# Performance work log

Measured on AMD Instinct MI355X. Metric: run time of the kernel, lower is better.

## Reference

```python
import jax, jax.numpy as jnp
import numpy as np

REG_MAX = 16
BOX_W = 7.5
OBJ_W = 1.0
TOPK = 10
EPS = 1e-7


def dfl_decode(x, reg_max):
    # x: [B, 4*reg_max, N] -> expected value of per-side distribution -> [B, N, 4] (xyxy)
    B, C, N = x.shape
    x = x.reshape(B, 4, reg_max, N)
    p = jax.nn.softmax(x, axis=2)
    proj = jnp.arange(reg_max, dtype=x.dtype)
    return jnp.einsum('bkrn,r->bnk', p, proj)


def bbox_ciou(b1, b2):
    # b1: [B,N,1,4], b2: [B,1,M,4], xyxy -> [B,N,M]
    x11, y11, x12, y12 = b1[..., 0], b1[..., 1], b1[..., 2], b1[..., 3]
    x21, y21, x22, y22 = b2[..., 0], b2[..., 1], b2[..., 2], b2[..., 3]
    w1, h1 = x12 - x11, y12 - y11
    w2, h2 = x22 - x21, y22 - y21
    iw = jnp.clip(jnp.minimum(x12, x22) - jnp.maximum(x11, x21), 0.0)
    ih = jnp.clip(jnp.minimum(y12, y22) - jnp.maximum(y11, y21), 0.0)
    inter = iw * ih
    union = w1 * h1 + w2 * h2 - inter + EPS
    iou = inter / union
    cw = jnp.maximum(x12, x22) - jnp.minimum(x11, x21)
    ch = jnp.maximum(y12, y22) - jnp.minimum(y11, y21)
    c2 = cw * cw + ch * ch + EPS
    rho2 = ((x21 + x22 - x11 - x12) ** 2 + (y21 + y22 - y11 - y12) ** 2) * 0.25
    v = (4.0 / (np.pi ** 2)) * (jnp.arctan(w2 / (h2 + EPS)) - jnp.arctan(w1 / (h1 + EPS))) ** 2
    alpha = jax.lax.stop_gradient(v / (v - iou + 1.0 + EPS))
    return iou - rho2 / c2 - alpha * v


def setup_inputs() -> dict:
    key = jax.random.key(0)
    k1, k2, k3, k4 = jax.random.split(key, 4)
    B, N, M = 8, 34000, 64
    boxes = jax.random.normal(k1, (B, 4 * REG_MAX, N), dtype=jnp.float32)
    scores = jax.random.normal(k2, (B, N), dtype=jnp.float32)
    # GT boxes: valid xyxy in roughly the same [0, reg_max) range as decoded preds
    xy = jax.random.uniform(k3, (B, M, 2), dtype=jnp.float32) * 11.0
    wh = jax.random.uniform(k4, (B, M, 2), dtype=jnp.float32) * 4.0 + 0.5
    targets = jnp.concatenate([xy, xy + wh], axis=-1)
    return {'boxes': boxes, 'scores': scores, 'targets': targets}


def reference(boxes, scores, targets):
    B, N = scores.shape
    M = targets.shape[1]
    pb = dfl_decode(boxes, REG_MAX)                     # [B,N,4]
    ciou = bbox_ciou(pb[:, :, None, :], targets[:, None, :, :])  # [B,N,M]
    k = min(TOPK, N)
    topv, topi = jax.lax.top_k(jnp.swapaxes(ciou, 1, 2), k)      # [B,M,k] over anchors
    valid = topv > 0.0
    vals = jnp.where(valid, topv, 0.0)

    def per_batch(idx, val, vld):
        flat_i = idx.reshape(-1)
        iou_t = jnp.zeros((N,), val.dtype).at[flat_i].max(val.reshape(-1))
        pos = jnp.zeros((N,), bool).at[flat_i].max(vld.reshape(-1))
        return iou_t, pos

    iou_target, pos = jax.vmap(per_batch)(topi, vals, valid)     # [B,N]
    posf = pos.astype(iou_target.dtype)
    npos = posf.sum(axis=1)
    box_per = jnp.where(npos > 0,
                        ((1.0 - iou_target) * posf).sum(axis=1) / jnp.maximum(npos, 1.0),
                        0.0)
    box_loss = box_per.sum()
    # BCEWithLogits (mean over anchors), summed over batch
    bce = jnp.maximum(scores, 0.0) - scores * iou_target + jnp.log1p(jnp.exp(-jnp.abs(scores)))
    obj_loss = bce.mean(axis=1).sum()
    total = (BOX_W * box_loss + OBJ_W * obj_loss) / B
    return total, box_loss, obj_loss
```

## Files before the change

kernel.cpp:

```cpp
#include <hip/hip_runtime.h>
#include <math.h>

#define BQ 8
#define MQ 64
#define REGMAX 16
#define KTOP 10
#define EPSQ 1e-7f
#define MBUF 1344

__device__ __forceinline__ float frcp(float x) { return __builtin_amdgcn_rcpf(x); }

#define ST_BYTES 256

__global__ __launch_bounds__(256) void decode_topk_kernel(
    const float* __restrict__ boxes, const float* __restrict__ scores,
    const float* __restrict__ targets, unsigned int* __restrict__ iou_bits,
    uint2* __restrict__ cand, float* __restrict__ acc, int N, int bpb) {
  const int tid = threadIdx.x;
  const int b = blockIdx.x / bpb;
  const int blk = blockIdx.x - b * bpb;
  const int a0 = blk * 256;
  const int w = tid >> 6;
  const int l = tid & 63;

  __shared__ float s_r1[5120];
  __shared__ float s_r2[1664];
  __shared__ int s_cnt;
  __shared__ float s_bce;
  float* stage = s_r1;
  float* s_hv = s_r1;
  int* s_hi = (int*)(s_r1 + 2560);
  float4* s_sv = (float4*)s_r2;
  float* s_at = s_r2 + 1024;
  int* s_ix = (int*)(s_r2 + 1280);
  uint2* s_mg = (uint2*)s_r2;

  if (tid == 0) { s_cnt = 0; s_bce = 0.f; }

  float out[4];
  const int c4 = a0 + l * 4;
  const bool cok = (c4 < N);
#pragma unroll
  for (int k = 0; k < 4; ++k) {
#pragma unroll
    for (int i = 0; i < 4; ++i) {
      const int r = w + i * 4;
      float4 v = make_float4(0.f, 0.f, 0.f, 0.f);
      if (cok)
        v = *(const float4*)&boxes[(size_t)(b * 64 + k * 16 + r) * (size_t)N + c4];
      *(float4*)&stage[r * 256 + l * 4] = v;
    }
    __syncthreads();
    float x[REGMAX];
#pragma unroll
    for (int r = 0; r < REGMAX; ++r) x[r] = stage[r * 256 + tid];
    float mx = x[0];
#pragma unroll
    for (int r = 1; r < REGMAX; ++r) mx = fmaxf(mx, x[r]);
    float s = 0.f, ws = 0.f;
#pragma unroll
    for (int r = 0; r < REGMAX; ++r) {
      float e = __expf(x[r] - mx);
      s += e;
      ws += (float)r * e;
    }
    out[k] = ws * frcp(s);
    __syncthreads();
  }

  const int n = a0 + tid;
  float bce0 = 0.f;
  if (n < N) {
    const size_t i = (size_t)b * N + n;
    iou_bits[i] = 0u;
    float sc = scores[i];
    bce0 = fmaxf(sc, 0.f) + log1pf(__expf(-fabsf(sc)));
    float x1 = out[0], y1 = out[1], x2 = out[2], y2 = out[3];
    float w1 = x2 - x1, h1 = y2 - y1;
    if (w1 > 0.f && h1 > 0.f) {
      int slot = atomicAdd(&s_cnt, 1);
      s_sv[slot] = make_float4(x1, y1, x2, y2);
      s_at[slot] = atanf(w1 * frcp(h1 + EPSQ));
      s_ix[slot] = n;
    }
  }
#pragma unroll
  for (int d = 1; d < 64; d <<= 1) bce0 += __shfl_xor(bce0, d, 64);
  if (l == 0) atomicAdd(&s_bce, bce0);
  __syncthreads();
  const int nsurv = s_cnt;
  if (tid == 0) atomicAdd(&acc[b * 4 + 2], s_bce);

  const float4 t = ((const float4*)targets)[b * MQ + l];
  const float x21 = t.x, y21 = t.y, x22 = t.z, y22 = t.w;
  const float w2 = x22 - x21, h2 = y22 - y21;
  const float atan_t = atanf(w2 * frcp(h2 + EPSQ));
  const float area2 = w2 * h2, sumx2 = x21 + x22, sumy2 = y21 + y22;
  const float CPI = 4.0f / (float)(M_PI * M_PI);

  float hv0 = 0.f, hv1 = 0.f, hv2 = 0.f, hv3 = 0.f, hv4 = 0.f;
  float hv5 = 0.f, hv6 = 0.f, hv7 = 0.f, hv8 = 0.f, hv9 = 0.f;
  int hi0 = 0, hi1 = 0, hi2 = 0, hi3 = 0, hi4 = 0;
  int hi5 = 0, hi6 = 0, hi7 = 0, hi8 = 0, hi9 = 0;

  const int qlen = (nsurv + 3) >> 2;
  const int j0 = w * qlen;
  const int j1 = min(nsurv, j0 + qlen);
  for (int j = j0; j < j1; ++j) {
    float4 p = s_sv[j];
    float pa = s_at[j];
    int ixj = s_ix[j];
    float x11 = p.x, y11 = p.y, x12 = p.z, y12 = p.w;
    float w1 = x12 - x11, h1 = y12 - y11;
    float iw = fmaxf(fminf(x12, x22) - fmaxf(x11, x21), 0.f);
    float ih = fmaxf(fminf(y12, y22) - fmaxf(y11, y21), 0.f);
    float inter = iw * ih;
    float uni = w1 * h1 + area2 - inter + EPSQ;
    float iou = inter * frcp(uni);
    float cw = fmaxf(x12, x22) - fminf(x11, x21);
    float ch = fmaxf(y12, y22) - fminf(y11, y21);
    float c2 = cw * cw + ch * ch + EPSQ;
    float dx = sumx2 - x11 - x12;
    float dy = sumy2 - y11 - y12;
    float rho2 = (dx * dx + dy * dy) * 0.25f;
    float da = atan_t - pa;
    float v = CPI * da * da;
    float alpha = v * frcp(v - iou + 1.f + EPSQ);
    float ciou = iou - rho2 * frcp(c2) - alpha * v;
    if (ciou > hv9) {
      float cv = ciou;
      int ci = ixj;
#define INS(vk, ik)                         \
  {                                         \
    bool gt = cv > vk;                      \
    float tv_ = vk; int ti_ = ik;           \
    vk = gt ? cv : vk; ik = gt ? ci : ik;   \
    cv = gt ? tv_ : cv; ci = gt ? ti_ : ci; \
  }
      INS(hv0, hi0) INS(hv1, hi1) INS(hv2, hi2) INS(hv3, hi3) INS(hv4, hi4)
      INS(hv5, hi5) INS(hv6, hi6) INS(hv7, hi7) INS(hv8, hi8) INS(hv9, hi9)
#undef INS
    }
  }
  const int hb = (w * MQ + l) * KTOP;
  s_hv[hb + 0] = hv0; s_hi[hb + 0] = hi0;
  s_hv[hb + 1] = hv1; s_hi[hb + 1] = hi1;
  s_hv[hb + 2] = hv2; s_hi[hb + 2] = hi2;
  s_hv[hb + 3] = hv3; s_hi[hb + 3] = hi3;
  s_hv[hb + 4] = hv4; s_hi[hb + 4] = hi4;
  s_hv[hb + 5] = hv5; s_hi[hb + 5] = hi5;
  s_hv[hb + 6] = hv6; s_hi[hb + 6] = hi6;
  s_hv[hb + 7] = hv7; s_hi[hb + 7] = hi7;
  s_hv[hb + 8] = hv8; s_hi[hb + 8] = hi8;
  s_hv[hb + 9] = hv9; s_hi[hb + 9] = hi9;
  __syncthreads();

  if (w == 0) {
    const int m = l;
    int p0 = 0, p1 = 0, p2 = 0, p3 = 0;
    for (int r = 0; r < KTOP; ++r) {
      float c0 = s_hv[(0 * MQ + m) * KTOP + p0];
      float c1 = s_hv[(1 * MQ + m) * KTOP + p1];
      float c2m = s_hv[(2 * MQ + m) * KTOP + p2];
      float c3 = s_hv[(3 * MQ + m) * KTOP + p3];
      float best = c0; int bw = 0;
      if (c1 > best) { best = c1; bw = 1; }
      if (c2m > best) { best = c2m; bw = 2; }
      if (c3 > best) { best = c3; bw = 3; }
      int psel = (bw == 0) ? p0 : (bw == 1) ? p1 : (bw == 2) ? p2 : p3;
      int bidx = s_hi[(bw * MQ + m) * KTOP + psel];
      s_mg[m * KTOP + r] = make_uint2(__float_as_uint(best), (unsigned)bidx);
      if (bw == 0) p0 = min(p0 + 1, KTOP - 1);
      else if (bw == 1) p1 = min(p1 + 1, KTOP - 1);
      else if (bw == 2) p2 = min(p2 + 1, KTOP - 1);
      else p3 = min(p3 + 1, KTOP - 1);
    }
  }
  __syncthreads();
  uint2* obase = cand + (size_t)(b * bpb + blk) * (MQ * KTOP);
  for (int sl = tid; sl < MQ * KTOP; sl += 256) obase[sl] = s_mg[sl];
}

__device__ __forceinline__ void select_top10(
    float* s_bv, int* s_bi, float* s_winv, int* s_wini,
    int* s_cnt, int c, int tid) {
  if (tid < 64) {
    for (int r = 0; r < KTOP; ++r) {
      float bv = 0.f;
      int bs = 0xffff;
      for (int sl = tid; sl < c; sl += 64) {
        float v = s_bv[sl];
        if (v > bv) { bv = v; bs = sl; }
      }
      unsigned long long key =
          ((unsigned long long)__float_as_uint(bv) << 32) | (unsigned int)bs;
#pragma unroll
      for (int d = 1; d < 64; d <<= 1) {
        unsigned long long o = __shfl_xor(key, d, 64);
        if (o > key) key = o;
      }
      if (tid == 0) {
        float wv = __uint_as_float((unsigned int)(key >> 32));
        int ws = (int)(key & 0xffffu);
        s_winv[r] = wv;
        if (wv > 0.f && ws != 0xffff) {
          s_wini[r] = s_bi[ws];
          s_bv[ws] = 0.f;
        } else {
          s_wini[r] = 0;
        }
      }
    }
    if (tid < KTOP) { s_bv[tid] = s_winv[tid]; s_bi[tid] = s_wini[tid]; }
    if (tid == 0) *s_cnt = KTOP;
  }
}

__global__ __launch_bounds__(256) void merge_kernel(
    const uint2* __restrict__ cand, const float* __restrict__ scores,
    unsigned int* __restrict__ iou_bits, float* __restrict__ acc,
    int N, int bpb) {
  const int bm = blockIdx.x;
  const int b = bm >> 6;
  const int m = bm & 63;
  const int tid = threadIdx.x;
  const int NC = bpb * KTOP;

  __shared__ float s_bv[MBUF];
  __shared__ int s_bi[MBUF];
  __shared__ float s_winv[KTOP];
  __shared__ int s_wini[KTOP];
  __shared__ int s_cnt;
  if (tid == 0) s_cnt = 0;
  __syncthreads();

  for (int k2 = tid; k2 < NC; k2 += 256) {
    int blkk = k2 / KTOP;
    int r = k2 - blkk * KTOP;
    uint2 e = cand[((size_t)(b * bpb + blkk) * MQ + m) * KTOP + r];
    float v = __uint_as_float(e.x);
    if (v > 0.f) {
      int slot = atomicAdd(&s_cnt, 1);
      s_bv[slot] = v;
      s_bi[slot] = (int)e.y;
    }
  }
  __syncthreads();
  int c = s_cnt;
  __syncthreads();
  if (c > KTOP) {
    select_top10(s_bv, s_bi, s_winv, s_wini, &s_cnt, c, tid);
    __syncthreads();
    c = KTOP;
  }
  if (tid < KTOP && tid < c) {
    float v = s_bv[tid];
    if (v > 0.f) {
      int ix = s_bi[tid];
      unsigned int vb = __float_as_uint(v);
      unsigned int old = atomicMax(&iou_bits[(size_t)b * N + ix], vb);
      if (old < vb) {
        float vold = __uint_as_float(old);
        bool was = (old != 0u);
        atomicAdd(&acc[b * 4 + 0], was ? (vold - v) : (1.f - v));
        if (!was) atomicAdd(&acc[b * 4 + 1], 1.f);
        atomicAdd(&acc[b * 4 + 2], -scores[(size_t)b * N + ix] * (v - vold));
      }
    }
  }
}

__global__ void finalize_kernel(const float* __restrict__ acc,
                                float* __restrict__ out, int N) {
  if (threadIdx.x == 0 && blockIdx.x == 0) {
    float box = 0.f, obj = 0.f;
    for (int bb = 0; bb < BQ; ++bb) {
      float sb = acc[bb * 4 + 0];
      float np = acc[bb * 4 + 1];
      float sc = acc[bb * 4 + 2];
      box += (np > 0.f) ? sb / fmaxf(np, 1.f) : 0.f;
      obj += sc / (float)N;
    }
    out[0] = (7.5f * box + obj) / (float)BQ;
    out[1] = box;
    out[2] = obj;
  }
}

extern "C" void kernel_launch(void* const* d_in, const int* in_sizes, int n_in,
                              void* d_out, int out_size, void* d_ws, size_t ws_size,
                              hipStream_t stream) {
  const float* boxes = (const float*)d_in[0];
  const float* scores = (const float*)d_in[1];
  const float* targets = (const float*)d_in[2];
  float* out = (float*)d_out;
  const int N = in_sizes[1] / BQ;

  const int bpb = (N + 255) / 256;

  char* ws = (char*)d_ws;
  size_t cand_bytes = (size_t)BQ * bpb * MQ * KTOP * sizeof(uint2);
  size_t iou_bytes = (size_t)BQ * N * sizeof(unsigned int);

  uint2* cand = (uint2*)ws;                    ws += cand_bytes;
  unsigned int* iou_bits = (unsigned int*)ws;  ws += iou_bytes;
  float* state = (float*)ws;

  hipMemsetAsync(state, 0, ST_BYTES, stream);

  decode_topk_kernel<<<BQ * bpb, 256, 0, stream>>>(boxes, scores, targets,
                                                   iou_bits, cand, state, N, bpb);
  merge_kernel<<<BQ * MQ, 256, 0, stream>>>(cand, scores, iou_bits, state, N, bpb);
  finalize_kernel<<<1, 64, 0, stream>>>(state, out, N);
}
```

Before: 143.1 us.

## Double-buffer DFL logits staging with async global-to-LDS loads

Replaces the synchronous global→register→LDS staging of each 16-row DFL slice with `global_load_lds` direct-to-LDS loads into two LDS buffers. The next side's slice is prefetched while the softmax expectation for the current side is computed. The aim is to overlap HBM latency with compute and drop the register round-trip. In exchange, LDS use grows to a separate 32KB staging region plus dedicated survivor arrays, which may lower occupancy. Tail columns are now clamped rather than zero-filled.

Measured after the change: 141.0 us. Within noise of the previous version (-1.4%).

```diff
diff --git a/kernel.cpp b/kernel.cpp
--- a/kernel.cpp
+++ b/kernel.cpp
@@ -11,6 +11,12 @@
 __device__ __forceinline__ float frcp(float x) { return __builtin_amdgcn_rcpf(x); }
 
 #define ST_BYTES 256
+
+__device__ __forceinline__ void async_row16(const float* g, float* lds) {
+  __builtin_amdgcn_global_load_lds(
+      (const __attribute__((address_space(1))) unsigned int*)(uintptr_t)g,
+      (__attribute__((address_space(3))) unsigned int*)(uintptr_t)lds, 16, 0, 0);
+}
 
 __global__ __launch_bounds__(256) void decode_topk_kernel(
     const float* __restrict__ boxes, const float* __restrict__ scores,
@@ -23,37 +29,47 @@
   const int w = tid >> 6;
   const int l = tid & 63;
 
-  __shared__ float s_r1[5120];
-  __shared__ float s_r2[1664];
+  __shared__ float s_u[8192];
+  float (*stage)[16][256] = (float (*)[16][256])s_u;
+  float* s_hv = s_u;
+  int* s_hi = (int*)(s_u + 2560);
+  uint2* s_mg = (uint2*)(s_u + 5120);
+
+  __shared__ float4 s_sv[256];
+  __shared__ float s_at[256];
+  __shared__ int s_ix[256];
   __shared__ int s_cnt;
   __shared__ float s_bce;
-  float* stage = s_r1;
-  float* s_hv = s_r1;
-  int* s_hi = (int*)(s_r1 + 2560);
-  float4* s_sv = (float4*)s_r2;
-  float* s_at = s_r2 + 1024;
-  int* s_ix = (int*)(s_r2 + 1280);
-  uint2* s_mg = (uint2*)s_r2;
-
   if (tid == 0) { s_cnt = 0; s_bce = 0.f; }
 
-  float out[4];
-  const int c4 = a0 + l * 4;
-  const bool cok = (c4 < N);
+  const size_t Ns = (size_t)N;
+  const int off = min(l * 4, N - a0 - 4);
+  const float* bbase = boxes + (size_t)(b * 64) * Ns + a0;
+
+  {
+#pragma unroll
+    for (int i = 0; i < 4; ++i) {
+      const int r = 4 * i + w;
+      async_row16(bbase + (size_t)r * Ns + off, &stage[0][r][0]);
+    }
+  }
+  __syncthreads();
+
+  float ev[4];
+  int buf = 0;
 #pragma unroll
   for (int k = 0; k < 4; ++k) {
-#pragma unroll
-    for (int i = 0; i < 4; ++i) {
-      const int r = w + i * 4;
-      float4 v = make_float4(0.f, 0.f, 0.f, 0.f);
-      if (cok)
-        v = *(const float4*)&boxes[(size_t)(b * 64 + k * 16 + r) * (size_t)N + c4];
-      *(float4*)&stage[r * 256 + l * 4] = v;
-    }
-    __syncthreads();
+    if (k < 3) {
+      const float* sb = bbase + (size_t)((k + 1) * 16) * Ns;
+#pragma unroll
+      for (int i = 0; i < 4; ++i) {
+        const int r = 4 * i + w;
+        async_row16(sb + (size_t)r * Ns + off, &stage[buf ^ 1][r][0]);
+      }
+    }
     float x[REGMAX];
 #pragma unroll
-    for (int r = 0; r < REGMAX; ++r) x[r] = stage[r * 256 + tid];
+    for (int r = 0; r < REGMAX; ++r) x[r] = stage[buf][r][tid];
     float mx = x[0];
 #pragma unroll
     for (int r = 1; r < REGMAX; ++r) mx = fmaxf(mx, x[r]);
@@ -64,8 +80,9 @@
       s += e;
       ws += (float)r * e;
     }
-    out[k] = ws * frcp(s);
+    ev[k] = ws * frcp(s);
     __syncthreads();
+    buf ^= 1;
   }
 
   const int n = a0 + tid;
@@ -75,11 +92,10 @@
     iou_bits[i] = 0u;
     float sc = scores[i];
     bce0 = fmaxf(sc, 0.f) + log1pf(__expf(-fabsf(sc)));
-    float x1 = out[0], y1 = out[1], x2 = out[2], y2 = out[3];
-    float w1 = x2 - x1, h1 = y2 - y1;
+    float w1 = ev[2] - ev[0], h1 = ev[3] - ev[1];
     if (w1 > 0.f && h1 > 0.f) {
       int slot = atomicAdd(&s_cnt, 1);
-      s_sv[slot] = make_float4(x1, y1, x2, y2);
+      s_sv[slot] = make_float4(ev[0], ev[1], ev[2], ev[3]);
       s_at[slot] = atanf(w1 * frcp(h1 + EPSQ));
       s_ix[slot] = n;
     }
```
